# Performance work log

Measured on AMD Instinct MI355X. Metric: run time of the kernel, lower is better.

Reference implementation:

```python
import jax, jax.numpy as jnp
import numpy as np

N = 100000
E = 3200000
IN_DIM = 64
HIDDEN = 128
NUM_CLASSES = 10


def setup_inputs() -> dict:
    key = jax.random.key(0)
    ks = jax.random.split(key, 12)
    x = jax.random.normal(ks[0], (N, IN_DIM), dtype=jnp.float32)
    edge_rows = jnp.sort(jax.random.randint(ks[1], (E,), 0, N, dtype=jnp.int32))
    edge_cols = jax.random.randint(ks[2], (E,), 0, N, dtype=jnp.int32)
    edge_vals = jax.random.uniform(ks[3], (E,), dtype=jnp.float32)
    s = 0.05
    fc1_w = jax.random.normal(ks[4], (IN_DIM, HIDDEN), dtype=jnp.float32) * s
    fc1_b = jnp.zeros((HIDDEN,), dtype=jnp.float32)
    fc2_w = jax.random.normal(ks[5], (HIDDEN, HIDDEN), dtype=jnp.float32) * s
    fc2_b = jnp.zeros((HIDDEN,), dtype=jnp.float32)
    att_w = jax.random.normal(ks[6], (HIDDEN, 1), dtype=jnp.float32) * s
    att_b = jnp.zeros((1,), dtype=jnp.float32)
    cls_w = jax.random.normal(ks[7], (HIDDEN, NUM_CLASSES), dtype=jnp.float32) * s
    cls_b = jnp.zeros((NUM_CLASSES,), dtype=jnp.float32)
    return {"x": x, "edge_rows": edge_rows, "edge_cols": edge_cols,
            "edge_vals": edge_vals, "fc1_w": fc1_w, "fc1_b": fc1_b,
            "fc2_w": fc2_w, "fc2_b": fc2_b, "att_w": att_w, "att_b": att_b,
            "cls_w": cls_w, "cls_b": cls_b}


def reference(x, edge_rows, edge_cols, edge_vals,
              fc1_w, fc1_b, fc2_w, fc2_b, att_w, att_b, cls_w, cls_b):
    n = x.shape[0]

    def spmm(mat):  # adj @ mat, adj in COO: out[r] += v * mat[c]
        return jax.ops.segment_sum(edge_vals[:, None] * mat[edge_cols],
                                   edge_rows, num_segments=n)

    h1 = jax.nn.relu(spmm(x @ fc1_w + fc1_b))          # [N, H]
    h2 = jax.nn.relu(spmm(h1 @ fc2_w + fc2_b))         # [N, H]
    h = h1 + h2
    w = jax.nn.softmax(h @ att_w + att_b, axis=0)      # [N, 1] softmax over nodes
    g = jnp.sum(w * h, axis=0)                         # [H]
    return g @ cls_w + cls_b                           # [num_classes]
```

## Files before the change

kernel.cpp:

```cpp
#include <hip/hip_runtime.h>
#include <hip/hip_bf16.h>
#include <math.h>


#define HID 128
#define NBA 1792
#define NW (NBA * 4)
#define NBC 128
#define NBT (NBA + NBC)

using short8 = __attribute__((ext_vector_type(8))) short;
using floatx4 = __attribute__((ext_vector_type(4))) float;

__device__ __forceinline__ float relu(float v) { return v > 0.f ? v : 0.f; }

__device__ __forceinline__ unsigned short f2bf(float f) {
  unsigned u = __float_as_uint(f);
  u += 0x7FFFu + ((u >> 16) & 1u);
  return (unsigned short)(u >> 16);
}
__device__ __forceinline__ float bflo(unsigned u) {
  return __uint_as_float(u << 16);
}
__device__ __forceinline__ float bfhi(unsigned u) {
  return __uint_as_float(u & 0xFFFF0000u);
}
__device__ __forceinline__ float bfu(unsigned short u) {
  return __uint_as_float((unsigned)u << 16);
}

__global__ __launch_bounds__(256) void prep_kernel(
    const float* __restrict__ x, const float* __restrict__ fc1w,
    const float* __restrict__ fc2w, unsigned char* __restrict__ xb,
    unsigned short* __restrict__ w1t, unsigned short* __restrict__ w2t,
    int n4) {
  const int b = blockIdx.x;
  const int t = threadIdx.x;
  if (b < 32) {
    int idx = b * 256 + t;
    int n = idx >> 6, k = idx & 63;
    w1t[idx] = f2bf(fc1w[k * 128 + n]);
  } else if (b < 96) {
    int idx = (b - 32) * 256 + t;
    int n = idx >> 7, k = idx & 127;
    w2t[idx] = f2bf(fc2w[k * 128 + n]);
  } else {
    int idx = (b - 96) * 256 + t;
    if (idx < n4) {
      float4 v = *(const float4*)&x[idx * 4];
      int w = __builtin_amdgcn_cvt_pk_fp8_f32(v.x, v.y, 0, false);
      w = __builtin_amdgcn_cvt_pk_fp8_f32(v.z, v.w, w, true);
      *(unsigned*)&xb[idx * 4] = (unsigned)w;
    }
  }
}

__global__ __launch_bounds__(256) void spmm1_kernel(
    const unsigned char* __restrict__ mat, const int* __restrict__ rows,
    const int* __restrict__ cols, const float* __restrict__ vals,
    float* __restrict__ ax, float* __restrict__ rs, int E) {
  int gw0 = (blockIdx.x * blockDim.x + threadIdx.x) >> 6;
  const int gw = __builtin_amdgcn_readfirstlane(gw0);
  const int lane = threadIdx.x & 63;
  const int nw = (gridDim.x * blockDim.x) >> 6;
  const int S = (E + nw - 1) / nw;
  int start = gw * S;
  int end = start + S;
  if (end > E) end = E;
  if (start >= end) return;

  float acc = 0.f, accv = 0.f;
  int curRow = rows[start];

  auto flush = [&]() {
    atomicAdd(ax + (size_t)curRow * 64 + lane, acc);
    if (lane == 0) atomicAdd(rs + curRow, accv);
    acc = 0.f;
    accv = 0.f;
  };

  for (int base = start; base < end; base += 64) {
    const int cnt = min(64, end - base);
    int c_ = 0, r_ = 0;
    float v_ = 0.f;
    if (lane < cnt) {
      int e = base + lane;
      c_ = __builtin_nontemporal_load(&cols[e]);
      v_ = __builtin_nontemporal_load(&vals[e]);
      r_ = __builtin_nontemporal_load(&rows[e]);
    }

    int j = 0;
    for (; j + 16 <= cnt; j += 16) {
      unsigned uu[16];
#pragma unroll
      for (int q = 0; q < 16; ++q) {
        int cq = __shfl(c_, j + q);
        uu[q] = mat[(unsigned)cq * 64u + (unsigned)lane];
      }
#pragma unroll
      for (int q = 0; q < 16; ++q) {
        float vq = __shfl(v_, j + q);
        int rq = __shfl(r_, j + q);
        if (rq != curRow) { flush(); curRow = rq; }
        acc = fmaf(vq, __builtin_amdgcn_cvt_f32_fp8(uu[q], 0), acc);
        accv += vq;
      }
    }
    for (; j < cnt; ++j) {
      int c = __shfl(c_, j);
      float v = __shfl(v_, j);
      int r = __shfl(r_, j);
      if (r != curRow) { flush(); curRow = r; }
      unsigned u = mat[(unsigned)c * 64u + (unsigned)lane];
      acc = fmaf(v, __builtin_amdgcn_cvt_f32_fp8(u, 0), acc);
      accv += v;
    }
  }
  flush();
}

#define A1S 88
#define H1S 136
__global__ __launch_bounds__(256) void fc_fused_kernel(
    const float* __restrict__ ax, const float* __restrict__ rs,
    const unsigned short* __restrict__ w1t, const float* __restrict__ b1,
    const unsigned short* __restrict__ w2t, const float* __restrict__ b2,
    unsigned short* __restrict__ h1r, unsigned char* __restrict__ t2,
    int N) {
  __shared__ unsigned short a1[64 * A1S];
  __shared__ unsigned short h1[64 * H1S];
  __shared__ float rsl[64];
  const int t = threadIdx.x;
  const int R0 = blockIdx.x * 64;

  const int limit = N * 64;
#pragma unroll
  for (int i = 0; i < 4; ++i) {
    int f = t * 4 + i * 1024;
    int g = R0 * 64 + f;
    float4 v = {0.f, 0.f, 0.f, 0.f};
    if (g < limit) v = *(const float4*)&ax[g];
    int row = f >> 6, k = f & 63;
    ushort4 o;
    o.x = f2bf(v.x); o.y = f2bf(v.y); o.z = f2bf(v.z); o.w = f2bf(v.w);
    *(ushort4*)&a1[row * A1S + k] = o;
  }
  if (t < 64) rsl[t] = (R0 + t < N) ? rs[R0 + t] : 0.f;
  __syncthreads();

  const int w = t >> 6, lane = t & 63;
  const int quad = lane >> 4, ln = lane & 15;
  const int m0 = w * 16;

  floatx4 acc[8];
#pragma unroll
  for (int nt = 0; nt < 8; ++nt) acc[nt] = {0.f, 0.f, 0.f, 0.f};
#pragma unroll
  for (int k0 = 0; k0 < 64; k0 += 32) {
    short8 af = *(short8*)&a1[(m0 + ln) * A1S + k0 + quad * 8];
#pragma unroll
    for (int nt = 0; nt < 8; ++nt) {
      short8 bf = *(const short8*)&w1t[(nt * 16 + ln) * 64 + k0 + quad * 8];
      acc[nt] = __builtin_amdgcn_mfma_f32_16x16x32_bf16(af, bf, acc[nt], 0, 0, 0);
    }
  }
  floatx4 rsv = *(floatx4*)&rsl[m0 + quad * 4];
#pragma unroll
  for (int nt = 0; nt < 8; ++nt) {
    float b1v = b1[nt * 16 + ln];
#pragma unroll
    for (int r = 0; r < 4; ++r) {
      float v = relu(acc[nt][r] + rsv[r] * b1v);
      h1[(m0 + quad * 4 + r) * H1S + nt * 16 + ln] = f2bf(v);
    }
  }
  {
    int rloc = m0 + (lane >> 2);
    int gr = R0 + rloc;
    int cq = (lane & 3) * 32;
    if (gr < N) {
#pragma unroll
      for (int j = 0; j < 4; ++j) {
        ushort4 lo = *(ushort4*)&h1[rloc * H1S + cq + j * 8];
        ushort4 hi = *(ushort4*)&h1[rloc * H1S + cq + j * 8 + 4];
        *(ushort4*)&h1r[(size_t)gr * HID + cq + j * 8] = lo;
        *(ushort4*)&h1r[(size_t)gr * HID + cq + j * 8 + 4] = hi;
      }
    }
  }

  floatx4 acc2[8];
#pragma unroll
  for (int nt = 0; nt < 8; ++nt) acc2[nt] = {0.f, 0.f, 0.f, 0.f};
#pragma unroll
  for (int k0 = 0; k0 < 128; k0 += 32) {
    short8 af = *(short8*)&h1[(m0 + ln) * H1S + k0 + quad * 8];
#pragma unroll
    for (int nt = 0; nt < 8; ++nt) {
      short8 bf = *(const short8*)&w2t[(nt * 16 + ln) * 128 + k0 + quad * 8];
      acc2[nt] = __builtin_amdgcn_mfma_f32_16x16x32_bf16(af, bf, acc2[nt], 0, 0, 0);
    }
  }
#pragma unroll
  for (int nt = 0; nt < 8; ++nt) {
    float b2v = b2[nt * 16 + ln];
#pragma unroll
    for (int r = 0; r < 4; ++r) {
      h1[(m0 + quad * 4 + r) * H1S + nt * 16 + ln] = f2bf(acc2[nt][r] + b2v);
    }
  }
  {
    int rloc = m0 + (lane >> 2);
    int gr = R0 + rloc;
    int cq = (lane & 3) * 32;
    if (gr < N) {
#pragma unroll
      for (int j = 0; j < 4; ++j) {
        ushort4 lo = *(ushort4*)&h1[rloc * H1S + cq + j * 8];
        ushort4 hi = *(ushort4*)&h1[rloc * H1S + cq + j * 8 + 4];
        int w0 = __builtin_amdgcn_cvt_pk_fp8_f32(bfu(lo.x), bfu(lo.y), 0, false);
        w0 = __builtin_amdgcn_cvt_pk_fp8_f32(bfu(lo.z), bfu(lo.w), w0, true);
        int w1 = __builtin_amdgcn_cvt_pk_fp8_f32(bfu(hi.x), bfu(hi.y), 0, false);
        w1 = __builtin_amdgcn_cvt_pk_fp8_f32(bfu(hi.z), bfu(hi.w), w1, true);
        uint2 o;
        o.x = (unsigned)w0;
        o.y = (unsigned)w1;
        *(uint2*)&t2[(size_t)gr * HID + cq + j * 8] = o;
      }
    }
  }
}

__global__ __launch_bounds__(256) void spmm2att_kernel(
    const unsigned char* __restrict__ mat, const unsigned short* __restrict__ h1r,
    const int* __restrict__ rows, const int* __restrict__ cols,
    const float* __restrict__ vals, const float* __restrict__ attw,
    const float* __restrict__ attb,
    int* __restrict__ rowF, int* __restrict__ rowL,
    float* __restrict__ dataF, float* __restrict__ dataL,
    float* __restrict__ pm, float* __restrict__ pden, float* __restrict__ pnum,
    int E, int S) {
  __shared__ float sm[4], sden[4], snum[4][HID];
  const int w = threadIdx.x >> 6;
  const int lane = threadIdx.x & 63;
  int ch0 = blockIdx.x * 4 + w;
  const int chunk = __builtin_amdgcn_readfirstlane(ch0);
  const int start = chunk * S;
  const int end = min(start + S, E);
  const int d2 = lane * 2;
  const float2 wv = *(const float2*)(attw + d2);
  const float battn = attb[0];

  float m = -INFINITY, den = 0.f, nx = 0.f, ny = 0.f;
  int fRow = -1, lRow = -1;

  if (start < end) {
    const int firstRow = rows[start];
    const bool cont = (start > 0) && (rows[start - 1] == firstRow);
    float2 acc = {0.f, 0.f};
    int curRow = firstRow;

    auto attproc = [&](int r, float2 a) {
      unsigned hu = *(const unsigned*)&h1r[(size_t)r * HID + d2];
      float hx = bflo(hu) + relu(a.x);
      float hy = bfhi(hu) + relu(a.y);
      float p = hx * wv.x + hy * wv.y;
#pragma unroll
      for (int off = 1; off < 64; off <<= 1) p += __shfl_xor(p, off);
      float sc = p + battn;
      if (sc > m) {
        float s = expf(m - sc);
        den *= s; nx *= s; ny *= s;
        m = sc;
      }
      float e = expf(sc - m);
      den += e;
      nx = fmaf(e, hx, nx);
      ny = fmaf(e, hy, ny);
    };
    auto emit = [&](int nextRow) {
      if (curRow == firstRow && cont) {
        *(float2*)&dataF[(size_t)chunk * HID + d2] = acc;
        fRow = curRow;
      } else {
        attproc(curRow, acc);
      }
      acc.x = acc.y = 0.f;
      curRow = nextRow;
    };

    for (int base = start; base < end; base += 64) {
      const int cnt = min(64, end - base);
      int c_ = 0, r_ = 0;
      float v_ = 0.f;
      if (lane < cnt) {
        int e = base + lane;
        c_ = __builtin_nontemporal_load(&cols[e]);
        v_ = __builtin_nontemporal_load(&vals[e]);
        r_ = __builtin_nontemporal_load(&rows[e]);
      }
      int j = 0;
      for (; j + 16 <= cnt; j += 16) {
        unsigned uu[16];
#pragma unroll
        for (int q = 0; q < 16; ++q) {
          int cq = __shfl(c_, j + q);
          uu[q] = *(const unsigned short*)(mat + (unsigned)cq * 128u +
                                           (unsigned)d2);
        }
#pragma unroll
        for (int q = 0; q < 16; ++q) {
          float vq = __shfl(v_, j + q);
          int rq = __shfl(r_, j + q);
          if (rq != curRow) emit(rq);
          acc.x = fmaf(vq, __builtin_amdgcn_cvt_f32_fp8(uu[q], 0), acc.x);
          acc.y = fmaf(vq, __builtin_amdgcn_cvt_f32_fp8(uu[q], 1), acc.y);
        }
      }
      for (; j < cnt; ++j) {
        int c = __shfl(c_, j);
        float v = __shfl(v_, j);
        int r = __shfl(r_, j);
        if (r != curRow) emit(r);
        unsigned u = *(const unsigned short*)(mat + (unsigned)c * 128u +
                                              (unsigned)d2);
        acc.x = fmaf(v, __builtin_amdgcn_cvt_f32_fp8(u, 0), acc.x);
        acc.y = fmaf(v, __builtin_amdgcn_cvt_f32_fp8(u, 1), acc.y);
      }
    }
    bool spanF = (end < E) && (rows[end] == curRow);
    if (curRow == firstRow && cont) {
      *(float2*)&dataF[(size_t)chunk * HID + d2] = acc;
      fRow = curRow;
    } else if (spanF) {
      *(float2*)&dataL[(size_t)chunk * HID + d2] = acc;
      lRow = curRow;
    } else {
      attproc(curRow, acc);
    }
  }
  if (lane == 0) { rowF[chunk] = fRow; rowL[chunk] = lRow; }

  if (lane == 0) { sm[w] = m; sden[w] = den; }
  snum[w][d2] = nx;
  snum[w][d2 + 1] = ny;
  __syncthreads();
  const int t = threadIdx.x;
  if (t < HID) {
    float M4 = fmaxf(fmaxf(sm[0], sm[1]), fmaxf(sm[2], sm[3]));
    float s0 = sden[0] > 0.f ? expf(sm[0] - M4) : 0.f;
    float s1 = sden[1] > 0.f ? expf(sm[1] - M4) : 0.f;
    float s2 = sden[2] > 0.f ? expf(sm[2] - M4) : 0.f;
    float s3 = sden[3] > 0.f ? expf(sm[3] - M4) : 0.f;
    pnum[(size_t)t * NBT + blockIdx.x] =
        snum[0][t] * s0 + snum[1][t] * s1 + snum[2][t] * s2 + snum[3][t] * s3;
    if (t == 0) {
      pden[blockIdx.x] = sden[0] * s0 + sden[1] * s1 + sden[2] * s2 + sden[3] * s3;
      pm[blockIdx.x] = M4;
    }
  }
}

__global__ __launch_bounds__(256) void att_cleanup_kernel(
    const unsigned short* __restrict__ h1r,
    const int* __restrict__ rowF, const int* __restrict__ rowL,
    const float* __restrict__ dataF, const float* __restrict__ dataL,
    const float* __restrict__ attw, const float* __restrict__ attb,
    float* __restrict__ pm, float* __restrict__ pden, float* __restrict__ pnum) {
  __shared__ float sm[4], sden[4], snum[4][HID];
  const int w = threadIdx.x >> 6;
  const int lane = threadIdx.x & 63;
  int wv0 = blockIdx.x * 4 + w;
  const int gwv = __builtin_amdgcn_readfirstlane(wv0);
  const int nw = NBC * 4;
  const int d2 = lane * 2;
  const float2 wvv = *(const float2*)(attw + d2);
  const float battn = attb[0];

  float m = -INFINITY, den = 0.f, nx = 0.f, ny = 0.f;
  for (int c = gwv; c < NW; c += nw) {
    int r = rowL[c];
    if (r < 0) continue;
    float2 acc = *(const float2*)&dataL[(size_t)c * HID + d2];
    int c2 = c + 1;
    while (c2 < NW && rowF[c2] == r) {
      float2 a2 = *(const float2*)&dataF[(size_t)c2 * HID + d2];
      acc.x += a2.x; acc.y += a2.y;
      ++c2;
    }
    unsigned hu = *(const unsigned*)&h1r[(size_t)r * HID + d2];
    float hx = bflo(hu) + relu(acc.x);
    float hy = bfhi(hu) + relu(acc.y);
    float p = hx * wvv.x + hy * wvv.y;
#pragma unroll
    for (int off = 1; off < 64; off <<= 1) p += __shfl_xor(p, off);
    float sc = p + battn;
    if (sc > m) {
      float s = expf(m - sc);
      den *= s; nx *= s; ny *= s;
      m = sc;
    }
    float e = expf(sc - m);
    den += e;
    nx = fmaf(e, hx, nx);
    ny = fmaf(e, hy, ny);
  }

  if (lane == 0) { sm[w] = m; sden[w] = den; }
  snum[w][d2] = nx;
  snum[w][d2 + 1] = ny;
  __syncthreads();
  const int t = threadIdx.x;
  if (t < HID) {
    float M4 = fmaxf(fmaxf(sm[0], sm[1]), fmaxf(sm[2], sm[3]));
    float s0 = sden[0] > 0.f ? expf(sm[0] - M4) : 0.f;
    float s1 = sden[1] > 0.f ? expf(sm[1] - M4) : 0.f;
    float s2 = sden[2] > 0.f ? expf(sm[2] - M4) : 0.f;
    float s3 = sden[3] > 0.f ? expf(sm[3] - M4) : 0.f;
    int pb = NBA + blockIdx.x;
    pnum[(size_t)t * NBT + pb] =
        snum[0][t] * s0 + snum[1][t] * s1 + snum[2][t] * s2 + snum[3][t] * s3;
    if (t == 0) {
      pden[pb] = sden[0] * s0 + sden[1] * s1 + sden[2] * s2 + sden[3] * s3;
      pm[pb] = M4;
    }
  }
}

__global__ __launch_bounds__(1024) void att_combine_kernel(
    const float* __restrict__ pm, const float* __restrict__ pden,
    const float* __restrict__ pnum, const float* __restrict__ clsw,
    const float* __restrict__ clsb, float* __restrict__ out) {
  __shared__ float red[1024];
  __shared__ float scale[NBT];
  __shared__ float g[HID + 1];
  const int t = threadIdx.x;

  float mloc = -INFINITY;
  for (int i = t; i < NBT; i += 1024) mloc = fmaxf(mloc, pm[i]);
  red[t] = mloc;
  __syncthreads();
  for (int off = 512; off > 0; off >>= 1) {
    if (t < off) red[t] = fmaxf(red[t], red[t + off]);
    __syncthreads();
  }
  const float M = red[0];
  __syncthreads();

  float dloc = 0.f;
  for (int i = t; i < NBT; i += 1024) {
    float dv = pden[i];
    float sc = dv > 0.f ? expf(pm[i] - M) : 0.f;
    scale[i] = sc;
    dloc += dv * sc;
  }
  red[t] = dloc;
  __syncthreads();
  for (int off = 512; off > 0; off >>= 1) {
    if (t < off) red[t] += red[t + off];
    __syncthreads();
  }
  if (t == 0) g[HID] = red[0];
  __syncthreads();

  const int c = t >> 3, bb = t & 7;
  float acc = 0.f;
  for (int i = bb; i < NBT; i += 8) acc += pnum[(size_t)c * NBT + i] * scale[i];
  acc += __shfl_down(acc, 4);
  acc += __shfl_down(acc, 2);
  acc += __shfl_down(acc, 1);
  if (bb == 0) g[c] = acc;
  __syncthreads();

  if (t < 10) {
    float o = 0.f;
    for (int d = 0; d < HID; ++d) o = fmaf(g[d], clsw[d * 10 + t], o);
    out[t] = clsb[t] + o / g[HID];
  }
}

extern "C" void kernel_launch(void* const* d_in, const int* in_sizes, int n_in,
                              void* d_out, int out_size, void* d_ws,
                              size_t ws_size, hipStream_t stream) {
  const float* x = (const float*)d_in[0];
  const int* erows = (const int*)d_in[1];
  const int* ecols = (const int*)d_in[2];
  const float* evals = (const float*)d_in[3];
  const float* fc1w = (const float*)d_in[4];
  const float* fc1b = (const float*)d_in[5];
  const float* fc2w = (const float*)d_in[6];
  const float* fc2b = (const float*)d_in[7];
  const float* attw = (const float*)d_in[8];
  const float* attb = (const float*)d_in[9];
  const float* clsw = (const float*)d_in[10];
  const float* clsb = (const float*)d_in[11];
  float* out = (float*)d_out;

  const int N = in_sizes[0] / 64;
  const int E = in_sizes[1];
  const int S = (E + NW - 1) / NW;

  char* p = (char*)d_ws;
  auto alloc = [&](size_t bytes) {
    char* q = p;
    p += (bytes + 255) & ~(size_t)255;
    return q;
  };
  unsigned char* xb = (unsigned char*)alloc((size_t)N * 64);
  float* ax = (float*)alloc((size_t)N * 64 * 4);
  float* rs = (float*)alloc((size_t)N * 4);
  unsigned short* h1r = (unsigned short*)alloc((size_t)N * HID * 2);
  unsigned char* t2 = (unsigned char*)alloc((size_t)N * HID);
  unsigned short* w1t = (unsigned short*)alloc(128 * 64 * 2);
  unsigned short* w2t = (unsigned short*)alloc(128 * 128 * 2);
  int* rowF2 = (int*)alloc(NW * 4);
  int* rowL2 = (int*)alloc(NW * 4);
  float* dataF2 = (float*)alloc((size_t)NW * HID * 4);
  float* dataL2 = (float*)alloc((size_t)NW * HID * 4);
  float* pm = (float*)alloc(NBT * 4);
  float* pden = (float*)alloc(NBT * 4);
  float* pnum = (float*)alloc((size_t)HID * NBT * 4);

  const int n4 = N * 16;
  const int nblk = (N + 63) / 64;

  hipMemsetAsync(ax, 0, (size_t)N * 65 * 4, stream);

  prep_kernel<<<96 + (n4 + 255) / 256, 256, 0, stream>>>(x, fc1w, fc2w, xb,
                                                         w1t, w2t, n4);
  spmm1_kernel<<<2048, 256, 0, stream>>>(xb, erows, ecols, evals, ax, rs, E);
  fc_fused_kernel<<<nblk, 256, 0, stream>>>(ax, rs, w1t, fc1b, w2t, fc2b,
                                            h1r, t2, N);
  spmm2att_kernel<<<NBA, 256, 0, stream>>>(t2, h1r, erows, ecols, evals,
                                           attw, attb, rowF2, rowL2,
                                           dataF2, dataL2, pm, pden, pnum,
                                           E, S);
  att_cleanup_kernel<<<NBC, 256, 0, stream>>>(h1r, rowF2, rowL2, dataF2,
                                              dataL2, attw, attb, pm, pden,
                                              pnum);
  att_combine_kernel<<<1, 1024, 0, stream>>>(pm, pden, pnum, clsw, clsb, out);
}
```

Baseline: 495.1 us.

## Gather FP8 rows with wide 8-byte loads and redistribute via cross-lane shuffles

Both SpMM gather loops switch from per-lane byte or short loads of each neighbour row to having each lane load 8 bytes, so a wave fetches 8 (first layer) or 4 (second layer) rows per load instruction. The needed element is then moved to its owning lane with shuffles and byte shifts. This cuts the number of memory instructions in the latency-bound gather. The cost is more shuffle/ALU work per edge and fewer loads in flight per batch (2 wide loads instead of 16 narrow ones).

```diff
diff --git a/kernel.cpp b/kernel.cpp
--- a/kernel.cpp
+++ b/kernel.cpp
@@ -69,6 +69,12 @@
   if (end > E) end = E;
   if (start >= end) return;
 
+  const int qsel = lane >> 3;
+  const unsigned off = ((unsigned)lane & 7u) * 8u;
+  const int srcb = lane >> 3;
+  const bool selhi = (lane >> 2) & 1;
+  const int sh8 = (lane & 3) * 8;
+
   float acc = 0.f, accv = 0.f;
   int curRow = rows[start];
 
@@ -77,6 +83,21 @@
     if (lane == 0) atomicAdd(rs + curRow, accv);
     acc = 0.f;
     accv = 0.f;
+  };
+
+  auto proc8 = [&](uint2 u, int j, int c_, float v_, int r_) {
+#pragma unroll
+    for (int q = 0; q < 8; ++q) {
+      int src = (q << 3) | srcb;
+      unsigned ux = (unsigned)__shfl((int)u.x, src);
+      unsigned uy = (unsigned)__shfl((int)u.y, src);
+      unsigned d = (selhi ? uy : ux) >> sh8;
+      float vq = __shfl(v_, j + q);
+      int rq = __shfl(r_, j + q);
+      if (rq != curRow) { flush(); curRow = rq; }
+      acc = fmaf(vq, __builtin_amdgcn_cvt_f32_fp8((int)d, 0), acc);
+      accv += vq;
+    }
   };
 
   for (int base = start; base < end; base += 64) {
@@ -92,20 +113,17 @@
 
     int j = 0;
     for (; j + 16 <= cnt; j += 16) {
-      unsigned uu[16];
-#pragma unroll
-      for (int q = 0; q < 16; ++q) {
-        int cq = __shfl(c_, j + q);
-        uu[q] = mat[(unsigned)cq * 64u + (unsigned)lane];
-      }
-#pragma unroll
-      for (int q = 0; q < 16; ++q) {
-        float vq = __shfl(v_, j + q);
-        int rq = __shfl(r_, j + q);
-        if (rq != curRow) { flush(); curRow = rq; }
-        acc = fmaf(vq, __builtin_amdgcn_cvt_f32_fp8(uu[q], 0), acc);
-        accv += vq;
-      }
+      unsigned ca = (unsigned)__shfl(c_, j + qsel);
+      unsigned cb = (unsigned)__shfl(c_, j + 8 + qsel);
+      uint2 ua = *(const uint2*)(mat + (size_t)(ca * 64u + off));
+      uint2 ub = *(const uint2*)(mat + (size_t)(cb * 64u + off));
+      proc8(ua, j, c_, v_, r_);
+      proc8(ub, j + 8, c_, v_, r_);
+    }
+    for (; j + 8 <= cnt; j += 8) {
+      unsigned ca = (unsigned)__shfl(c_, j + qsel);
+      uint2 ua = *(const uint2*)(mat + (size_t)(ca * 64u + off));
+      proc8(ua, j, c_, v_, r_);
     }
     for (; j < cnt; ++j) {
       int c = __shfl(c_, j);
@@ -113,7 +131,7 @@
       int r = __shfl(r_, j);
       if (r != curRow) { flush(); curRow = r; }
       unsigned u = mat[(unsigned)c * 64u + (unsigned)lane];
-      acc = fmaf(v, __builtin_amdgcn_cvt_f32_fp8(u, 0), acc);
+      acc = fmaf(v, __builtin_amdgcn_cvt_f32_fp8((int)u, 0), acc);
       accv += v;
     }
   }
@@ -252,6 +270,12 @@
   const float2 wv = *(const float2*)(attw + d2);
   const float battn = attb[0];
 
+  const int qsel = lane >> 4;
+  const unsigned off = ((unsigned)lane & 15u) * 8u;
+  const int srcb = lane >> 2;
+  const bool selhi = (lane >> 1) & 1;
+  const int sh16 = (lane & 1) * 16;
+
   float m = -INFINITY, den = 0.f, nx = 0.f, ny = 0.f;
   int fRow = -1, lRow = -1;
 
@@ -267,7 +291,7 @@
       float hy = bfhi(hu) + relu(a.y);
       float p = hx * wv.x + hy * wv.y;
 #pragma unroll
-      for (int off = 1; off < 64; off <<= 1) p += __shfl_xor(p, off);
+      for (int off2 = 1; off2 < 64; off2 <<= 1) p += __shfl_xor(p, off2);
       float sc = p + battn;
       if (sc > m) {
         float s = expf(m - sc);
@@ -290,6 +314,21 @@
       curRow = nextRow;
     };
 
+    auto proc4 = [&](uint2 u, int j, float v_, int r_) {
+#pragma unroll
+      for (int q = 0; q < 4; ++q) {
+        int src = (q << 4) | srcb;
+        unsigned ux = (unsigned)__shfl((int)u.x, src);
+        unsigned uy = (unsigned)__shfl((int)u.y, src);
+        unsigned d = (selhi ? uy : ux) >> sh16;
+        float vq = __shfl(v_, j + q);
+        int rq = __shfl(r_, j + q);
+        if (rq != curRow) emit(rq);
+        acc.x = fmaf(vq, __builtin_amdgcn_cvt_f32_fp8((int)d, 0), acc.x);
+        acc.y = fmaf(vq, __builtin_amdgcn_cvt_f32_fp8((int)d, 1), acc.y);
+      }
+    };
+
     for (int base = start; base < end; base += 64) {
       const int cnt = min(64, end - base);
       int c_ = 0, r_ = 0;
@@ -301,22 +340,18 @@
         r_ = __builtin_nontemporal_load(&rows[e]);
       }
       int j = 0;
-      for (; j + 16 <= cnt; j += 16) {
-        unsigned uu[16];
-#pragma unroll
-        for (int q = 0; q < 16; ++q) {
-          int cq = __shfl(c_, j + q);
-          uu[q] = *(const unsigned short*)(mat + (unsigned)cq * 128u +
-                                           (unsigned)d2);
-        }
-#pragma unroll
-        for (int q = 0; q < 16; ++q) {
-          float vq = __shfl(v_, j + q);
-          int rq = __shfl(r_, j + q);
-          if (rq != curRow) emit(rq);
-          acc.x = fmaf(vq, __builtin_amdgcn_cvt_f32_fp8(uu[q], 0), acc.x);
-          acc.y = fmaf(vq, __builtin_amdgcn_cvt_f32_fp8(uu[q], 1), acc.y);
-        }
+      for (; j + 8 <= cnt; j += 8) {
+        unsigned ca = (unsigned)__shfl(c_, j + qsel);
+        unsigned cb = (unsigned)__shfl(c_, j + 4 + qsel);
+        uint2 ua = *(const uint2*)(mat + (size_t)(ca * 128u + off));
+        uint2 ub = *(const uint2*)(mat + (size_t)(cb * 128u + off));
+        proc4(ua, j, v_, r_);
+        proc4(ub, j + 4, v_, r_);
+      }
+      for (; j + 4 <= cnt; j += 4) {
+        unsigned ca = (unsigned)__shfl(c_, j + qsel);
+        uint2 ua = *(const uint2*)(mat + (size_t)(ca * 128u + off));
+        proc4(ua, j, v_, r_);
       }
       for (; j < cnt; ++j) {
         int c = __shfl(c_, j);
@@ -325,8 +360,8 @@
         if (r != curRow) emit(r);
         unsigned u = *(const unsigned short*)(mat + (unsigned)c * 128u +
                                               (unsigned)d2);
-        acc.x = fmaf(v, __builtin_amdgcn_cvt_f32_fp8(u, 0), acc.x);
-        acc.y = fmaf(v, __builtin_amdgcn_cvt_f32_fp8(u, 1), acc.y);
+        acc.x = fmaf(v, __builtin_amdgcn_cvt_f32_fp8((int)u, 0), acc.x);
+        acc.y = fmaf(v, __builtin_amdgcn_cvt_f32_fp8((int)u, 1), acc.y);
       }
     }
     bool spanF = (end < E) && (rows[end] == curRow);
```

Result: slower. 566.7 us (+14.4%).
